# Performance work log

Measured on AMD Instinct MI355X. Metric: run time of the kernel, lower is better.

## Reference

```python
import jax, jax.numpy as jnp
import numpy as np

ALPHA = 0.2

def setup_inputs() -> dict:
    key = jax.random.key(0)
    k1, k2, k3, k4 = jax.random.split(key, 4)
    B, S, I, H, O = 64, 2048, 128, 512, 64
    x = jax.random.normal(k1, (B, S, I), dtype=jnp.float32)
    # weights pre-transposed: y = x @ W (torch Linear uses x @ W.T)
    Wih = jax.random.normal(k2, (I, H), dtype=jnp.float32) / np.sqrt(I)
    W_rec = jax.random.normal(k3, (H, H), dtype=jnp.float32) / np.sqrt(H)
    Who = jax.random.normal(k4, (H, O), dtype=jnp.float32) / np.sqrt(H)
    return {"x": x, "Wih": Wih, "W_rec": W_rec, "Who": Who}

def reference(x, Wih, W_rec, Who):
    B, S, _ = x.shape
    H = W_rec.shape[0]
    u = jnp.einsum('bsi,ih->bsh', x, Wih)          # input projection, done once
    u_t = jnp.transpose(u, (1, 0, 2))              # [S, B, H] for scan
    h0 = jnp.zeros((B, H), dtype=x.dtype)          # initial_state=None -> zeros

    def step(h, u_step):
        r = jnp.tanh(u_step + h @ W_rec)           # eval mode: no noise
        h_new = (1.0 - ALPHA) * h + ALPHA * r      # leaky integration
        return h_new, h_new

    _, hs = jax.lax.scan(step, h0, u_t)            # hs: [S, B, H]
    out = jnp.einsum('sbh,ho->bso', hs, Who)       # readout, batched GEMM
    return out
```

## Files before the change

kernel.cpp:

```cpp
#include <hip/hip_runtime.h>
#include <hip/hip_fp16.h>
#include <cstdint>
#include <cstddef>

typedef _Float16 f16;
typedef _Float16 f16x2 __attribute__((ext_vector_type(2)));
typedef _Float16 f16x4 __attribute__((ext_vector_type(4)));
typedef _Float16 f16x8 __attribute__((ext_vector_type(8)));
typedef int i32x4 __attribute__((ext_vector_type(4)));

#define S_LEN 2048
#define BATCH 64
#define I_DIM 128
#define H_DIM 512
#define O_DIM 64

__device__ __forceinline__ float fdot2f(f16x2 a, f16x2 b, float c) {
#if __has_builtin(__builtin_amdgcn_fdot2)
    return __builtin_amdgcn_fdot2(a, b, c, false);
#else
    return c + (float)a.x * (float)b.x + (float)a.y * (float)b.y;
#endif
}

__global__ __launch_bounds__(256)
void u_gemm_kernel(const float* __restrict__ x, const float* __restrict__ Wih,
                   f16* __restrict__ u) {
    const int tid = threadIdx.x;
    const int r0 = blockIdx.x * 32;
    const int c0 = blockIdx.y * 128;

    __shared__ __align__(16) f16x2 wih_s[I_DIM / 2][128];
    __shared__ __align__(16) f16x2 x_s[32][I_DIM / 2];

#pragma unroll
    for (int i = 0; i < 32; ++i) {
        int idx = i * 256 + tid;
        int kp = idx >> 7;
        int cl = idx & 127;
        float w0 = Wih[(size_t)(2 * kp + 0) * H_DIM + c0 + cl];
        float w1 = Wih[(size_t)(2 * kp + 1) * H_DIM + c0 + cl];
        f16x2 w; w.x = (f16)w0; w.y = (f16)w1;
        wih_s[kp][cl] = w;
    }
    const float4* xs = (const float4*)(x + (size_t)r0 * I_DIM);
    f16x4* xd = (f16x4*)x_s;
#pragma unroll
    for (int i = 0; i < 4; ++i) {
        int idx = i * 256 + tid;
        float4 v = xs[idx];
        f16x4 h; h.x = (f16)v.x; h.y = (f16)v.y; h.z = (f16)v.z; h.w = (f16)v.w;
        xd[idx] = h;
    }
    __syncthreads();

    const int cl = tid & 127;
    const int rh = tid >> 7;
    float acc[16];
#pragma unroll
    for (int r = 0; r < 16; ++r) acc[r] = 0.f;

#pragma unroll
    for (int kc = 0; kc < 2; ++kc) {
        f16x2 wv[32];
#pragma unroll
        for (int i = 0; i < 32; ++i) wv[i] = wih_s[kc * 32 + i][cl];
#pragma unroll
        for (int r = 0; r < 16; ++r) {
            const int row = rh * 16 + r;
#pragma unroll
            for (int m = 0; m < 8; ++m) {
                f16x8 h8v = *(const f16x8*)(&x_s[row][kc * 32 + 4 * m]);
                const f16x2* hp = (const f16x2*)&h8v;
                acc[r] = fdot2f(wv[4 * m + 0], hp[0], acc[r]);
                acc[r] = fdot2f(wv[4 * m + 1], hp[1], acc[r]);
                acc[r] = fdot2f(wv[4 * m + 2], hp[2], acc[r]);
                acc[r] = fdot2f(wv[4 * m + 3], hp[3], acc[r]);
            }
        }
    }
#pragma unroll
    for (int r = 0; r < 16; ++r) {
        int row = r0 + rh * 16 + r;
        u[(size_t)row * H_DIM + c0 + cl] = (f16)acc[r];
    }
}

__global__ __launch_bounds__(512, 2)
void rnn_scan_kernel(const float* __restrict__ Wrec, f16* __restrict__ uhs) {
    const int tid = threadIdx.x;
    const int b = blockIdx.x;
    const int l = tid & 63;
    const int w = tid >> 6;
    const int grp = l >> 4;
    const int li = l & 15;

    __shared__ __align__(16) signed char h8[2][512];
    __shared__ float colmax[512];

    {
        const float* wp = Wrec + tid;
        float m0 = 0.f, m1 = 0.f, m2 = 0.f, m3 = 0.f;
        for (int k = 0; k < 512; k += 4) {
            m0 = fmaxf(m0, __builtin_fabsf(wp[(size_t)(k + 0) * H_DIM]));
            m1 = fmaxf(m1, __builtin_fabsf(wp[(size_t)(k + 1) * H_DIM]));
            m2 = fmaxf(m2, __builtin_fabsf(wp[(size_t)(k + 2) * H_DIM]));
            m3 = fmaxf(m3, __builtin_fabsf(wp[(size_t)(k + 3) * H_DIM]));
        }
        float m = fmaxf(fmaxf(m0, m1), fmaxf(m2, m3));
        colmax[tid] = fmaxf(m, 1e-20f);
    }
    h8[0][tid & 511] = 0;
    __syncthreads();

    i32x4 wf[8][4];
#pragma unroll
    for (int j = 0; j < 4; ++j) {
        const int col = w * 64 + j * 16 + li;
        const float* wp = Wrec + col;
        const float sc = 127.f / colmax[col];
#pragma unroll
        for (int kt = 0; kt < 8; ++kt) {
            int wd0 = 0, wd1 = 0, wd2 = 0, wd3 = 0;
#pragma unroll
            for (int jj = 0; jj < 16; ++jj) {
                float v = wp[(size_t)(kt * 64 + grp * 16 + jj) * H_DIM] * sc;
                v = fminf(fmaxf(v, -127.f), 127.f);
                int q = ((int)rintf(v)) & 255;
                int sh = 8 * (jj & 3);
                if (jj < 4)       wd0 |= q << sh;
                else if (jj < 8)  wd1 |= q << sh;
                else if (jj < 12) wd2 |= q << sh;
                else              wd3 |= q << sh;
            }
            i32x4 f; f.x = wd0; f.y = wd1; f.z = wd2; f.w = wd3;
            wf[kt][j] = f;
        }
    }

    f16* io = uhs + (size_t)b * S_LEN * H_DIM + tid;
    const float inv = colmax[tid] * (1.f / 16129.f);

    float hp = 0.f;
    float uc = (float)io[0];
    f16 ua = (f16)0.f;
    if (S_LEN > 1) ua = io[H_DIM];

    __syncthreads();

    for (int t = 0; t < S_LEN; ++t) {
        f16 ub = (f16)0.f;
        if (t + 2 < S_LEN) ub = io[(size_t)(t + 2) * H_DIM];

        const signed char* hb = h8[t & 1];
        i32x4 av[8];
#pragma unroll
        for (int kt = 0; kt < 8; ++kt)
            av[kt] = *(const i32x4*)(hb + kt * 64 + grp * 16);

        i32x4 a0 = {0,0,0,0}, a1 = {0,0,0,0}, a2 = {0,0,0,0}, a3 = {0,0,0,0};
#pragma unroll
        for (int kt = 0; kt < 8; ++kt) {
            a0 = __builtin_amdgcn_mfma_i32_16x16x64_i8(av[kt], wf[kt][0], a0, 0, 0, 0);
            a1 = __builtin_amdgcn_mfma_i32_16x16x64_i8(av[kt], wf[kt][1], a1, 0, 0, 0);
            a2 = __builtin_amdgcn_mfma_i32_16x16x64_i8(av[kt], wf[kt][2], a2, 0, 0, 0);
            a3 = __builtin_amdgcn_mfma_i32_16x16x64_i8(av[kt], wf[kt][3], a3, 0, 0, 0);
        }

        int zi = grp == 0 ? a0[0] : grp == 1 ? a1[0] : grp == 2 ? a2[0] : a3[0];
        float z = (float)zi * inv + uc;

        float e2 = __expf(2.f * z);
        float r = 1.f - 2.f * __builtin_amdgcn_rcpf(e2 + 1.f);
        hp = 0.8f * hp + 0.2f * r;

        h8[(t + 1) & 1][tid] = (signed char)(int)rintf(hp * 127.f);
        io[(size_t)t * H_DIM] = (f16)hp;

        uc = (float)ua;
        ua = ub;
        __syncthreads();
    }
}

__global__ __launch_bounds__(256)
void out_gemm_kernel(const f16* __restrict__ hs, const float* __restrict__ Who,
                     float* __restrict__ out) {
    const int tid = threadIdx.x;
    const int r0 = blockIdx.x * 32;

    __shared__ __align__(16) f16x2 who_s[128][O_DIM];
    __shared__ __align__(16) f16x2 hs_s[32][128];

    const int o = tid & 63;
    const int rg = tid >> 6;

    float acc[8];
#pragma unroll
    for (int r = 0; r < 8; ++r) acc[r] = 0.f;

    for (int kc = 0; kc < 2; ++kc) {
        if (kc) __syncthreads();
#pragma unroll
        for (int i = 0; i < 32; ++i) {
            int idx = i * 256 + tid;
            int kp = idx >> 6;
            int oc = idx & 63;
            float w0 = Who[(size_t)(kc * 256 + 2 * kp + 0) * O_DIM + oc];
            float w1 = Who[(size_t)(kc * 256 + 2 * kp + 1) * O_DIM + oc];
            f16x2 wv2; wv2.x = (f16)w0; wv2.y = (f16)w1;
            who_s[kp][oc] = wv2;
        }
        f16x8* hd = (f16x8*)hs_s;
#pragma unroll
        for (int i = 0; i < 4; ++i) {
            int idx = i * 256 + tid;
            int r = idx >> 5;
            int m = idx & 31;
            f16x8 v = *(const f16x8*)(hs + (size_t)(r0 + r) * H_DIM + kc * 256 + m * 8);
            hd[idx] = v;
        }
        __syncthreads();

#pragma unroll
        for (int sc = 0; sc < 4; ++sc) {
            f16x2 wv[32];
#pragma unroll
            for (int i = 0; i < 32; ++i) wv[i] = who_s[sc * 32 + i][o];
#pragma unroll
            for (int r = 0; r < 8; ++r) {
                const int row = rg * 8 + r;
#pragma unroll
                for (int m = 0; m < 8; ++m) {
                    f16x8 h8v = *(const f16x8*)(&hs_s[row][sc * 32 + 4 * m]);
                    const f16x2* hp = (const f16x2*)&h8v;
                    acc[r] = fdot2f(wv[4 * m + 0], hp[0], acc[r]);
                    acc[r] = fdot2f(wv[4 * m + 1], hp[1], acc[r]);
                    acc[r] = fdot2f(wv[4 * m + 2], hp[2], acc[r]);
                    acc[r] = fdot2f(wv[4 * m + 3], hp[3], acc[r]);
                }
            }
        }
    }
#pragma unroll
    for (int r = 0; r < 8; ++r) {
        int row = r0 + rg * 8 + r;
        out[(size_t)row * O_DIM + o] = acc[r];
    }
}

extern "C" void kernel_launch(void* const* d_in, const int* in_sizes, int n_in,
                              void* d_out, int out_size, void* d_ws, size_t ws_size,
                              hipStream_t stream) {
    const float* x    = (const float*)d_in[0];
    const float* Wih  = (const float*)d_in[1];
    const float* Wrec = (const float*)d_in[2];
    const float* Who  = (const float*)d_in[3];
    float* out = (float*)d_out;
    f16* uhs = (f16*)d_ws;

    const int R = BATCH * S_LEN;

    u_gemm_kernel<<<dim3(R / 32, H_DIM / 128), 256, 0, stream>>>(x, Wih, uhs);
    rnn_scan_kernel<<<dim3(BATCH), 512, 0, stream>>>(Wrec, uhs);
    out_gemm_kernel<<<dim3(R / 32), 256, 0, stream>>>(uhs, Who, out);
}
```

Measured before the change: 1.905 ms.

## Replace per-step int8 MFMA matvec with sdot4 k-split and DPP reduction

The recurrent matvec in the scan kernel now has each thread hold a 4-column by 128-k int8 slice of W_rec in registers and accumulate with packed sdot4 instructions. Partial sums from the four k-groups are combined with quad DPP shuffles, in place of 16x16x64 MFMAs whose batch dimension was wasted on a single batch row. The hidden-state buffer is split into padded per-k-group slices to avoid LDS bank conflicts. This cuts the wasted MFMA work per timestep in exchange for more VALU instructions and 128 weight registers per thread.

```diff
diff --git a/kernel.cpp b/kernel.cpp
--- a/kernel.cpp
+++ b/kernel.cpp
@@ -21,6 +21,26 @@
 #else
     return c + (float)a.x * (float)b.x + (float)a.y * (float)b.y;
 #endif
+}
+
+__device__ __forceinline__ int sdot4(int a, int b, int c) {
+#if __has_builtin(__builtin_amdgcn_sdot4)
+    return __builtin_amdgcn_sdot4(a, b, c, false);
+#else
+    int r = c;
+#pragma unroll
+    for (int i = 0; i < 4; ++i) {
+        int av = (a << (24 - 8 * i)) >> 24;
+        int bv = (b << (24 - 8 * i)) >> 24;
+        r += av * bv;
+    }
+    return r;
+#endif
+}
+
+template <int CTRL>
+__device__ __forceinline__ int dpp_qi(int v) {
+    return __builtin_amdgcn_update_dpp(0, v, CTRL, 0xF, 0xF, true);
 }
 
 __global__ __launch_bounds__(256)
@@ -86,16 +106,16 @@
     }
 }
 
+#define SLICE_STRIDE 144
+
 __global__ __launch_bounds__(512, 2)
 void rnn_scan_kernel(const float* __restrict__ Wrec, f16* __restrict__ uhs) {
     const int tid = threadIdx.x;
     const int b = blockIdx.x;
-    const int l = tid & 63;
-    const int w = tid >> 6;
-    const int grp = l >> 4;
-    const int li = l & 15;
-
-    __shared__ __align__(16) signed char h8[2][512];
+    const int kg = tid & 3;
+    const int cq = tid >> 2;
+
+    __shared__ __align__(16) signed char h8[2][4 * SLICE_STRIDE];
     __shared__ float colmax[512];
 
     {
@@ -110,36 +130,33 @@
         float m = fmaxf(fmaxf(m0, m1), fmaxf(m2, m3));
         colmax[tid] = fmaxf(m, 1e-20f);
     }
-    h8[0][tid & 511] = 0;
+    h8[0][tid] = 0;
+    if (tid < 4 * SLICE_STRIDE - 512) h8[0][512 + tid] = 0;
     __syncthreads();
 
-    i32x4 wf[8][4];
-#pragma unroll
-    for (int j = 0; j < 4; ++j) {
-        const int col = w * 64 + j * 16 + li;
+    int wq[32][4];
+#pragma unroll
+    for (int i = 0; i < 4; ++i) {
+        const int col = cq + 128 * i;
         const float* wp = Wrec + col;
         const float sc = 127.f / colmax[col];
 #pragma unroll
-        for (int kt = 0; kt < 8; ++kt) {
-            int wd0 = 0, wd1 = 0, wd2 = 0, wd3 = 0;
-#pragma unroll
-            for (int jj = 0; jj < 16; ++jj) {
-                float v = wp[(size_t)(kt * 64 + grp * 16 + jj) * H_DIM] * sc;
+        for (int q = 0; q < 32; ++q) {
+            int wd = 0;
+#pragma unroll
+            for (int e = 0; e < 4; ++e) {
+                float v = wp[(size_t)(kg * 128 + 4 * q + e) * H_DIM] * sc;
                 v = fminf(fmaxf(v, -127.f), 127.f);
-                int q = ((int)rintf(v)) & 255;
-                int sh = 8 * (jj & 3);
-                if (jj < 4)       wd0 |= q << sh;
-                else if (jj < 8)  wd1 |= q << sh;
-                else if (jj < 12) wd2 |= q << sh;
-                else              wd3 |= q << sh;
-            }
-            i32x4 f; f.x = wd0; f.y = wd1; f.z = wd2; f.w = wd3;
-            wf[kt][j] = f;
-        }
-    }
-
-    f16* io = uhs + (size_t)b * S_LEN * H_DIM + tid;
-    const float inv = colmax[tid] * (1.f / 16129.f);
+                wd |= (((int)rintf(v)) & 255) << (8 * e);
+            }
+            wq[q][i] = wd;
+        }
+    }
+
+    const int jk = (kg + (cq & 3)) & 3;
+    const int c_own = cq + 128 * jk;
+    f16* io = uhs + (size_t)b * S_LEN * H_DIM + c_own;
+    const float inv = colmax[c_own] * (1.f / 16129.f);
 
     float hp = 0.f;
     float uc = (float)io[0];
@@ -152,29 +169,40 @@
         f16 ub = (f16)0.f;
         if (t + 2 < S_LEN) ub = io[(size_t)(t + 2) * H_DIM];
 
-        const signed char* hb = h8[t & 1];
+        const signed char* hb = h8[t & 1] + kg * SLICE_STRIDE;
         i32x4 av[8];
 #pragma unroll
-        for (int kt = 0; kt < 8; ++kt)
-            av[kt] = *(const i32x4*)(hb + kt * 64 + grp * 16);
-
-        i32x4 a0 = {0,0,0,0}, a1 = {0,0,0,0}, a2 = {0,0,0,0}, a3 = {0,0,0,0};
-#pragma unroll
-        for (int kt = 0; kt < 8; ++kt) {
-            a0 = __builtin_amdgcn_mfma_i32_16x16x64_i8(av[kt], wf[kt][0], a0, 0, 0, 0);
-            a1 = __builtin_amdgcn_mfma_i32_16x16x64_i8(av[kt], wf[kt][1], a1, 0, 0, 0);
-            a2 = __builtin_amdgcn_mfma_i32_16x16x64_i8(av[kt], wf[kt][2], a2, 0, 0, 0);
-            a3 = __builtin_amdgcn_mfma_i32_16x16x64_i8(av[kt], wf[kt][3], a3, 0, 0, 0);
-        }
-
-        int zi = grp == 0 ? a0[0] : grp == 1 ? a1[0] : grp == 2 ? a2[0] : a3[0];
+        for (int m = 0; m < 8; ++m)
+            av[m] = *(const i32x4*)(hb + 16 * m);
+
+        int ac0 = 0, ac1 = 0, ac2 = 0, ac3 = 0;
+#pragma unroll
+        for (int m = 0; m < 8; ++m) {
+#pragma unroll
+            for (int d = 0; d < 4; ++d) {
+                const int q = 4 * m + d;
+                const int hv = av[m][d];
+                ac0 = sdot4(hv, wq[q][0], ac0);
+                ac1 = sdot4(hv, wq[q][1], ac1);
+                ac2 = sdot4(hv, wq[q][2], ac2);
+                ac3 = sdot4(hv, wq[q][3], ac3);
+            }
+        }
+
+        ac0 += dpp_qi<0xB1>(ac0);  ac1 += dpp_qi<0xB1>(ac1);
+        ac2 += dpp_qi<0xB1>(ac2);  ac3 += dpp_qi<0xB1>(ac3);
+        ac0 += dpp_qi<0x4E>(ac0);  ac1 += dpp_qi<0x4E>(ac1);
+        ac2 += dpp_qi<0x4E>(ac2);  ac3 += dpp_qi<0x4E>(ac3);
+
+        int zi = jk == 0 ? ac0 : jk == 1 ? ac1 : jk == 2 ? ac2 : ac3;
         float z = (float)zi * inv + uc;
 
         float e2 = __expf(2.f * z);
         float r = 1.f - 2.f * __builtin_amdgcn_rcpf(e2 + 1.f);
         hp = 0.8f * hp + 0.2f * r;
 
-        h8[(t + 1) & 1][tid] = (signed char)(int)rintf(hp * 127.f);
+        h8[(t + 1) & 1][jk * SLICE_STRIDE + cq] =
+            (signed char)(int)rintf(hp * 127.f);
         io[(size_t)t * H_DIM] = (f16)hp;
 
         uc = (float)ua;
```

After: 2.108 ms. +10.7%, slower.

## Rewrite input projection GEMM with MFMA 16x16x32 f16 and swizzled LDS

Applied to the files above, without the earlier changes.

Replaces the fdot2-based input projection kernel with one using MFMA 16x16x32 f16 instructions. The weight tile is stored transposed in LDS with an XOR swizzle to avoid bank conflicts, and x rows are loaded straight into registers as A fragments. Each block now covers 64 rows instead of 32. The scan kernel, which likely dominates total time, is essentially unchanged, so the overall gain is limited to the projection stage.

```diff
diff --git a/kernel.cpp b/kernel.cpp
--- a/kernel.cpp
+++ b/kernel.cpp
@@ -8,6 +8,7 @@
 typedef _Float16 f16x4 __attribute__((ext_vector_type(4)));
 typedef _Float16 f16x8 __attribute__((ext_vector_type(8)));
 typedef int i32x4 __attribute__((ext_vector_type(4)));
+typedef float f32x4 __attribute__((ext_vector_type(4)));
 
 #define S_LEN 2048
 #define BATCH 64
@@ -27,62 +28,60 @@
 void u_gemm_kernel(const float* __restrict__ x, const float* __restrict__ Wih,
                    f16* __restrict__ u) {
     const int tid = threadIdx.x;
-    const int r0 = blockIdx.x * 32;
+    const int lane = tid & 63;
+    const int w = tid >> 6;
+    const int li = lane & 15;
+    const int g = lane >> 4;
+    const size_t r0 = (size_t)blockIdx.x * 64;
     const int c0 = blockIdx.y * 128;
 
-    __shared__ __align__(16) f16x2 wih_s[I_DIM / 2][128];
-    __shared__ __align__(16) f16x2 x_s[32][I_DIM / 2];
-
-#pragma unroll
-    for (int i = 0; i < 32; ++i) {
+    __shared__ __align__(16) f16 bT[128 * 128];
+
+#pragma unroll
+    for (int i = 0; i < 64; ++i) {
         int idx = i * 256 + tid;
-        int kp = idx >> 7;
-        int cl = idx & 127;
-        float w0 = Wih[(size_t)(2 * kp + 0) * H_DIM + c0 + cl];
-        float w1 = Wih[(size_t)(2 * kp + 1) * H_DIM + c0 + cl];
-        f16x2 w; w.x = (f16)w0; w.y = (f16)w1;
-        wih_s[kp][cl] = w;
-    }
-    const float4* xs = (const float4*)(x + (size_t)r0 * I_DIM);
-    f16x4* xd = (f16x4*)x_s;
-#pragma unroll
-    for (int i = 0; i < 4; ++i) {
-        int idx = i * 256 + tid;
-        float4 v = xs[idx];
-        f16x4 h; h.x = (f16)v.x; h.y = (f16)v.y; h.z = (f16)v.z; h.w = (f16)v.w;
-        xd[idx] = h;
+        int k = idx >> 7;
+        int c = idx & 127;
+        float v = Wih[(size_t)k * H_DIM + c0 + c];
+        bT[c * 128 + (k ^ ((c & 7) << 3))] = (f16)v;
+    }
+
+    const int tr = (int)r0 + w * 16 + li;
+    f16x8 a[4];
+#pragma unroll
+    for (int kt = 0; kt < 4; ++kt) {
+        const float* xp = x + (size_t)tr * I_DIM + kt * 32 + g * 8;
+        f32x4 v0 = *(const f32x4*)(xp);
+        f32x4 v1 = *(const f32x4*)(xp + 4);
+        f16x8 h;
+        h[0] = (f16)v0[0]; h[1] = (f16)v0[1]; h[2] = (f16)v0[2]; h[3] = (f16)v0[3];
+        h[4] = (f16)v1[0]; h[5] = (f16)v1[1]; h[6] = (f16)v1[2]; h[7] = (f16)v1[3];
+        a[kt] = h;
     }
     __syncthreads();
 
-    const int cl = tid & 127;
-    const int rh = tid >> 7;
-    float acc[16];
-#pragma unroll
-    for (int r = 0; r < 16; ++r) acc[r] = 0.f;
-
-#pragma unroll
-    for (int kc = 0; kc < 2; ++kc) {
-        f16x2 wv[32];
-#pragma unroll
-        for (int i = 0; i < 32; ++i) wv[i] = wih_s[kc * 32 + i][cl];
-#pragma unroll
-        for (int r = 0; r < 16; ++r) {
-            const int row = rh * 16 + r;
-#pragma unroll
-            for (int m = 0; m < 8; ++m) {
-                f16x8 h8v = *(const f16x8*)(&x_s[row][kc * 32 + 4 * m]);
-                const f16x2* hp = (const f16x2*)&h8v;
-                acc[r] = fdot2f(wv[4 * m + 0], hp[0], acc[r]);
-                acc[r] = fdot2f(wv[4 * m + 1], hp[1], acc[r]);
-                acc[r] = fdot2f(wv[4 * m + 2], hp[2], acc[r]);
-                acc[r] = fdot2f(wv[4 * m + 3], hp[3], acc[r]);
-            }
-        }
-    }
-#pragma unroll
-    for (int r = 0; r < 16; ++r) {
-        int row = r0 + rh * 16 + r;
-        u[(size_t)row * H_DIM + c0 + cl] = (f16)acc[r];
+    f32x4 acc[8];
+#pragma unroll
+    for (int n = 0; n < 8; ++n) acc[n] = (f32x4){0.f, 0.f, 0.f, 0.f};
+
+#pragma unroll
+    for (int kt = 0; kt < 4; ++kt) {
+#pragma unroll
+        for (int n = 0; n < 8; ++n) {
+            const int c = n * 16 + li;
+            const int koff = (kt * 32 + g * 8) ^ ((c & 7) << 3);
+            f16x8 b = *(const f16x8*)(&bT[c * 128 + koff]);
+            acc[n] = __builtin_amdgcn_mfma_f32_16x16x32_f16(a[kt], b, acc[n], 0, 0, 0);
+        }
+    }
+
+#pragma unroll
+    for (int n = 0; n < 8; ++n) {
+#pragma unroll
+        for (int r = 0; r < 4; ++r) {
+            size_t row = r0 + w * 16 + g * 4 + r;
+            u[row * H_DIM + c0 + n * 16 + li] = (f16)acc[n][r];
+        }
     }
 }
 
@@ -110,7 +109,7 @@
         float m = fmaxf(fmaxf(m0, m1), fmaxf(m2, m3));
         colmax[tid] = fmaxf(m, 1e-20f);
     }
-    h8[0][tid & 511] = 0;
+    h8[0][tid] = 0;
     __syncthreads();
 
     i32x4 wf[8][4];
@@ -261,7 +260,7 @@
 
     const int R = BATCH * S_LEN;
 
-    u_gemm_kernel<<<dim3(R / 32, H_DIM / 128), 256, 0, stream>>>(x, Wih, uhs);
+    u_gemm_kernel<<<dim3(R / 64, H_DIM / 128), 256, 0, stream>>>(x, Wih, uhs);
     rnn_scan_kernel<<<dim3(BATCH), 512, 0, stream>>>(Wrec, uhs);
     out_gemm_kernel<<<dim3(R / 32), 256, 0, stream>>>(uhs, Who, out);
 }
```

Result: faster. 1.761 ms (-7.6%).
